# Kernel tuning notes

Hardware: AMD Instinct MI355X
Metric: run time of the kernel (lower is better)

The kernel has to match this reference:

```python
import jax, jax.numpy as jnp
import numpy as np

B, T, D_EMB, D_QKV = 8, 2048, 1024, 64
SCALE = 1.0 / (D_QKV ** 0.5)


def setup_inputs() -> dict:
    key = jax.random.key(0)
    kx, kq, kk, kv = jax.random.split(key, 4)
    return {
        "x": jax.random.normal(kx, (B, T, D_EMB), dtype=jnp.float32),
        "Wq": jax.random.normal(kq, (D_EMB, D_QKV), dtype=jnp.float32) * 0.02,
        "Wk": jax.random.normal(kk, (D_EMB, D_QKV), dtype=jnp.float32) * 0.02,
        "Wv": jax.random.normal(kv, (D_EMB, D_QKV), dtype=jnp.float32) * 0.02,
    }


def reference(x, Wq, Wk, Wv):
    # x: [B, T, D_emb]; projections to [B, T, D_qkv]
    q = jnp.einsum("bte,ed->btd", x, Wq)
    k = jnp.einsum("bte,ed->btd", x, Wk)
    v = jnp.einsum("bte,ed->btd", x, Wv)
    # scores: [B, T, T], scaled then causally masked
    scores = jnp.einsum("bqd,bkd->bqk", q, k) * SCALE
    t = x.shape[1]
    causal = jnp.tril(jnp.ones((t, t), dtype=bool))
    scores = jnp.where(causal[None, :, :], scores, -jnp.inf)
    attn = jax.nn.softmax(scores, axis=-1)
    return jnp.einsum("bqk,bkd->bqd", attn, v)
```

## Files before the change

kernel.cpp:

```cpp
#include <hip/hip_runtime.h>

typedef float f32x4 __attribute__((ext_vector_type(4)));
typedef __bf16 bf16x8 __attribute__((ext_vector_type(8)));
typedef __bf16 bf16x4 __attribute__((ext_vector_type(4)));

#define T_ 2048
#define DE 1024
#define DQ 64
#define SCALE 0.125f

#define GL16(gp, lp)                                                        \
  __builtin_amdgcn_global_load_lds(                                         \
      (const __attribute__((address_space(1))) void*)(gp),                  \
      (__attribute__((address_space(3))) void*)(lp), 16, 0, 0)

#define WAITVM0 asm volatile("s_waitcnt vmcnt(0)" ::: "memory")

__global__ __launch_bounds__(256) void kw_pack(
    const float* __restrict__ Wq, const float* __restrict__ Wk,
    const float* __restrict__ Wv, __bf16* __restrict__ Wf)
{
  int tid = blockIdx.x * 256 + threadIdx.x;
  int lane = tid & 63, f = tid >> 6;
  int t = f % 12, kc = f / 12;
  const float* W = (t < 4) ? Wq : ((t < 8) ? Wk : Wv);
  int nl = (t & 3) * 16 + (lane & 15);
  int k0 = kc * 32 + (lane >> 4) * 8;
  bf16x8 v;
#pragma unroll
  for (int j = 0; j < 8; ++j) v[j] = (__bf16)W[(size_t)(k0 + j) * 64 + nl];
  *(bf16x8*)(Wf + (size_t)tid * 8) = v;
}

__global__ __launch_bounds__(256) void kproj(
    const float* __restrict__ x, const __bf16* __restrict__ Wf,
    __bf16* __restrict__ Qb, __bf16* __restrict__ Kb, __bf16* __restrict__ Vt)
{
  __shared__ char lds[2][32768];
  const int tid = threadIdx.x;
  const int lane = tid & 63;
  const int w = tid >> 6;
  const int col = lane & 15, g = lane >> 4;
  const int msub = w & 1;
  const int ng = w >> 1;
  const int mbase = blockIdx.x * 32;

  size_t gbase[8];
  int gstride[8], ldst[8];
#pragma unroll
  for (int cc = 0; cc < 2; ++cc) {
    int q = w * 2 + cc;
    int row = q * 4 + (lane >> 4);
    int kbyte = ((lane & 15) * 16) ^ ((row & 7) << 4);
    gbase[cc] = (size_t)(mbase + row) * 4096 + (size_t)kbyte;
    gstride[cc] = 256;
    ldst[cc] = q * 1024 + lane * 16;
  }
#pragma unroll
  for (int cc = 2; cc < 8; ++cc) {
    int j = w * 6 + cc - 2;
    gbase[cc] = (size_t)j * 1024 + (size_t)lane * 16;
    gstride[cc] = 24576;
    ldst[cc] = 8192 + j * 1024 + lane * 16;
  }

  f32x4 acc[6];
#pragma unroll
  for (int i = 0; i < 6; ++i) acc[i] = (f32x4){0.f, 0.f, 0.f, 0.f};

  const char* xb = (const char*)x;
  const char* wb = (const char*)Wf;

#define STAGE(ks, bi)                                                       \
  {                                                                         \
    char* lb = &lds[bi][0];                                                 \
    _Pragma("unroll")                                                       \
    for (int cc = 0; cc < 2; ++cc)                                          \
      GL16(xb + gbase[cc] + (size_t)(ks) * gstride[cc], lb + ldst[cc]);     \
    _Pragma("unroll")                                                       \
    for (int cc = 2; cc < 8; ++cc)                                          \
      GL16(wb + gbase[cc] + (size_t)(ks) * gstride[cc], lb + ldst[cc]);     \
  }

#define KSTEP(ks, bi)                                                       \
  {                                                                         \
    const char* la = &lds[bi][0];                                           \
    const char* lbB = &lds[bi][8192];                                       \
    const int arow = msub * 16 + col;                                       \
    const char* abase = la + arow * 256;                                    \
    const int sw = (arow & 7) << 4;                                         \
    _Pragma("unroll")                                                       \
    for (int kh = 0; kh < 2; ++kh) {                                        \
      int kb = kh * 128 + g * 32;                                           \
      f32x4 a0 = *(const f32x4*)(abase + (kb ^ sw));                        \
      f32x4 a1 = *(const f32x4*)(abase + ((kb + 16) ^ sw));                 \
      bf16x8 af;                                                            \
      _Pragma("unroll")                                                     \
      for (int j = 0; j < 4; ++j) { af[j] = (__bf16)a0[j]; af[4 + j] = (__bf16)a1[j]; } \
      _Pragma("unroll")                                                     \
      for (int ii = 0; ii < 6; ++ii) {                                      \
        int nt = ng * 6 + ii;                                               \
        bf16x8 bfr = *(const bf16x8*)(lbB + ((kh * 12 + nt) * 64 + lane) * 16); \
        acc[ii] = __builtin_amdgcn_mfma_f32_16x16x32_bf16(af, bfr, acc[ii], 0, 0, 0); \
      }                                                                     \
    }                                                                       \
  }

  STAGE(0, 0);
  for (int ks = 0; ks < 16; ++ks) {
    WAITVM0;
    __builtin_amdgcn_s_barrier();
    __builtin_amdgcn_sched_barrier(0);
    if (ks < 15) STAGE(ks + 1, (ks + 1) & 1);
    KSTEP(ks, ks & 1);
  }

#undef STAGE
#undef KSTEP

  const int b = mbase >> 11;
  const int mrow = mbase + msub * 16 + g * 4;
  const int trow = (mbase & 2047) + msub * 16 + g * 4;
#pragma unroll
  for (int ii = 0; ii < 6; ++ii) {
    int ti = ng * 6 + ii;
    if (ti < 8) {
      __bf16* dst = (ti < 4) ? Qb : Kb;
      int c = (ti & 3) * 16 + col;
#pragma unroll
      for (int r = 0; r < 4; ++r)
        dst[(size_t)(mrow + r) * DQ + c] = (__bf16)acc[ii][r];
    } else {
      int d = (ti - 8) * 16 + col;
      bf16x4 v;
#pragma unroll
      for (int r = 0; r < 4; ++r) v[r] = (__bf16)acc[ii][r];
      *(bf16x4*)(Vt + ((size_t)(b * DQ + d)) * T_ + trow) = v;
    }
  }
}

__global__ __launch_bounds__(256) void kattn(
    const __bf16* __restrict__ Qb, const __bf16* __restrict__ Kb,
    const __bf16* __restrict__ Vt, float* __restrict__ out)
{
  __shared__ float accs[4][32][68];
  __shared__ float mls[4][2][32];
  __shared__ __bf16 plds[4][2][16][72];

  const int tid = threadIdx.x;
  const int lane = tid & 63;
  const int w = tid >> 6;
  const int col = lane & 15, g = lane >> 4;
  const int b = blockIdx.x & 7;
  const int jq = 63 - (blockIdx.x >> 3);
  const int qbase = jq * 32;

  bf16x8 qa[2][2];
#pragma unroll
  for (int mt = 0; mt < 2; ++mt) {
    const __bf16* Qp = Qb + (size_t)(b * T_ + qbase + mt * 16 + col) * DQ + g * 8;
    qa[mt][0] = *(const bf16x8*)(Qp);
    qa[mt][1] = *(const bf16x8*)(Qp + 32);
  }

  const __bf16* Kbb = Kb + (size_t)b * T_ * DQ;
  const __bf16* Vbb = Vt + (size_t)b * DQ * T_;

  f32x4 acc[2][4];
#pragma unroll
  for (int mt = 0; mt < 2; ++mt)
#pragma unroll
    for (int dt = 0; dt < 4; ++dt) acc[mt][dt] = (f32x4){0.f,0.f,0.f,0.f};
  float mrun[2][4], lsum[2][4];
#pragma unroll
  for (int mt = 0; mt < 2; ++mt)
#pragma unroll
    for (int r = 0; r < 4; ++r) { mrun[mt][r] = -1e30f; lsum[mt][r] = 0.f; }

  const int nb = (jq >> 1) + 1;
  for (int it = w; it < nb; it += 4) {
    const int nbase = it * 64;

    bf16x8 kf_[4][2];
#pragma unroll
    for (int nt = 0; nt < 4; ++nt) {
      const __bf16* Kp = Kbb + (size_t)(nbase + nt * 16 + col) * DQ + g * 8;
      kf_[nt][0] = *(const bf16x8*)(Kp);
      kf_[nt][1] = *(const bf16x8*)(Kp + 32);
    }

    f32x4 s[2][4];
#pragma unroll
    for (int mt = 0; mt < 2; ++mt)
#pragma unroll
      for (int nt = 0; nt < 4; ++nt) {
        f32x4 t = __builtin_amdgcn_mfma_f32_16x16x32_bf16(qa[mt][0], kf_[nt][0],
                                                          (f32x4){0.f,0.f,0.f,0.f}, 0, 0, 0);
        s[mt][nt] = __builtin_amdgcn_mfma_f32_16x16x32_bf16(qa[mt][1], kf_[nt][1], t, 0, 0, 0);
      }

    bf16x8 vf[4][2];
#pragma unroll
    for (int dt = 0; dt < 4; ++dt) {
      const __bf16* Vp = Vbb + (size_t)(dt * 16 + col) * T_ + nbase + g * 8;
      vf[dt][0] = *(const bf16x8*)(Vp);
      vf[dt][1] = *(const bf16x8*)(Vp + 32);
    }

#pragma unroll
    for (int mt = 0; mt < 2; ++mt)
#pragma unroll
      for (int nt = 0; nt < 4; ++nt)
#pragma unroll
        for (int r = 0; r < 4; ++r) s[mt][nt][r] *= SCALE;
    if (it == nb - 1) {
#pragma unroll
      for (int mt = 0; mt < 2; ++mt)
#pragma unroll
        for (int nt = 0; nt < 4; ++nt)
#pragma unroll
          for (int r = 0; r < 4; ++r)
            if (nbase + nt * 16 + col > qbase + mt * 16 + g * 4 + r) s[mt][nt][r] = -1e30f;
    }

    float mv[2][4];
#pragma unroll
    for (int mt = 0; mt < 2; ++mt)
#pragma unroll
      for (int r = 0; r < 4; ++r)
        mv[mt][r] = fmaxf(fmaxf(s[mt][0][r], s[mt][1][r]), fmaxf(s[mt][2][r], s[mt][3][r]));
#pragma unroll
    for (int sh = 1; sh <= 8; sh <<= 1)
#pragma unroll
      for (int mt = 0; mt < 2; ++mt)
#pragma unroll
        for (int r = 0; r < 4; ++r) mv[mt][r] = fmaxf(mv[mt][r], __shfl_xor(mv[mt][r], sh, 64));

#pragma unroll
    for (int mt = 0; mt < 2; ++mt)
#pragma unroll
      for (int r = 0; r < 4; ++r) {
        float mn = fmaxf(mrun[mt][r], mv[mt][r]);
        float rs = __expf(mrun[mt][r] - mn);
        mrun[mt][r] = mn;
        float ps = 0.f;
#pragma unroll
        for (int nt = 0; nt < 4; ++nt) {
          s[mt][nt][r] = __expf(s[mt][nt][r] - mn);
          ps += s[mt][nt][r];
        }
        lsum[mt][r] = lsum[mt][r] * rs + ps;
#pragma unroll
        for (int dt = 0; dt < 4; ++dt) acc[mt][dt][r] *= rs;
      }

#pragma unroll
    for (int mt = 0; mt < 2; ++mt)
#pragma unroll
      for (int nt = 0; nt < 4; ++nt)
#pragma unroll
        for (int r = 0; r < 4; ++r)
          plds[w][mt][g * 4 + r][nt * 16 + col] = (__bf16)s[mt][nt][r];

    bf16x8 pa[2][2];
#pragma unroll
    for (int mt = 0; mt < 2; ++mt) {
      pa[mt][0] = *(const bf16x8*)&plds[w][mt][col][g * 8];
      pa[mt][1] = *(const bf16x8*)&plds[w][mt][col][32 + g * 8];
    }

#pragma unroll
    for (int mt = 0; mt < 2; ++mt)
#pragma unroll
      for (int dt = 0; dt < 4; ++dt) {
        f32x4 t = __builtin_amdgcn_mfma_f32_16x16x32_bf16(pa[mt][0], vf[dt][0], acc[mt][dt], 0, 0, 0);
        acc[mt][dt] = __builtin_amdgcn_mfma_f32_16x16x32_bf16(pa[mt][1], vf[dt][1], t, 0, 0, 0);
      }
  }

#pragma unroll
  for (int sh = 1; sh <= 8; sh <<= 1)
#pragma unroll
    for (int mt = 0; mt < 2; ++mt)
#pragma unroll
      for (int r = 0; r < 4; ++r) lsum[mt][r] += __shfl_xor(lsum[mt][r], sh, 64);

#pragma unroll
  for (int mt = 0; mt < 2; ++mt)
#pragma unroll
    for (int r = 0; r < 4; ++r) {
      int row = mt * 16 + g * 4 + r;
      accs[w][row][col]      = acc[mt][0][r];
      accs[w][row][col + 16] = acc[mt][1][r];
      accs[w][row][col + 32] = acc[mt][2][r];
      accs[w][row][col + 48] = acc[mt][3][r];
      if (col == 0) { mls[w][0][row] = mrun[mt][r]; mls[w][1][row] = lsum[mt][r]; }
    }
  __syncthreads();

#pragma unroll
  for (int pass = 0; pass < 2; ++pass) {
    int row = pass * 16 + (tid >> 4);
    int c4 = (tid & 15) * 4;
    float m0 = mls[0][0][row], m1 = mls[1][0][row];
    float m2 = mls[2][0][row], m3 = mls[3][0][row];
    float M = fmaxf(fmaxf(m0, m1), fmaxf(m2, m3));
    float s0 = __expf(m0 - M), s1 = __expf(m1 - M);
    float s2 = __expf(m2 - M), s3 = __expf(m3 - M);
    float L = s0 * mls[0][1][row] + s1 * mls[1][1][row]
            + s2 * mls[2][1][row] + s3 * mls[3][1][row];
    f32x4 a0 = *(const f32x4*)&accs[0][row][c4];
    f32x4 a1 = *(const f32x4*)&accs[1][row][c4];
    f32x4 a2 = *(const f32x4*)&accs[2][row][c4];
    f32x4 a3 = *(const f32x4*)&accs[3][row][c4];
    float inv = 1.f / L;
    f32x4 o;
#pragma unroll
    for (int j = 0; j < 4; ++j)
      o[j] = (s0 * a0[j] + s1 * a1[j] + s2 * a2[j] + s3 * a3[j]) * inv;
    *(f32x4*)(out + (size_t)(b * T_ + qbase + row) * DQ + c4) = o;
  }
}

extern "C" void kernel_launch(void* const* d_in, const int* in_sizes, int n_in,
                              void* d_out, int out_size, void* d_ws, size_t ws_size,
                              hipStream_t stream)
{
  const float* x  = (const float*)d_in[0];
  const float* Wq = (const float*)d_in[1];
  const float* Wk = (const float*)d_in[2];
  const float* Wv = (const float*)d_in[3];
  float* out = (float*)d_out;

  char* ws = (char*)d_ws;
  __bf16* Wf = (__bf16*)(ws);
  __bf16* Qb = (__bf16*)(ws + 0x80000);
  __bf16* Kb = (__bf16*)(ws + 0x80000 + 0x200000);
  __bf16* Vt = (__bf16*)(ws + 0x80000 + 0x400000);

  kw_pack<<<96, 256, 0, stream>>>(Wq, Wk, Wv, Wf);
  kproj<<<512, 256, 0, stream>>>(x, Wf, Qb, Kb, Vt);
  kattn<<<512, 256, 0, stream>>>(Qb, Kb, Vt, out);
}
```

Before: 51.66 us.

## Triple-buffer x tiles and prefetch two steps ahead in projection kernel

Splits the projection kernel's LDS staging into a 3-deep ring for the x activation tiles and a 2-deep ring for the packed weight tiles. Each iteration waits only until the older loads finish (vmcnt 2) rather than draining all outstanding loads. This lets the x loads for step ks+2 stay in flight while step ks computes, hiding more global latency. The cost is more LDS per block (72KB vs 64KB), which may reduce occupancy, and a fully unrolled loop with fixed wait counts.

```diff
diff --git a/kernel.cpp b/kernel.cpp
--- a/kernel.cpp
+++ b/kernel.cpp
@@ -14,7 +14,7 @@
       (const __attribute__((address_space(1))) void*)(gp),                  \
       (__attribute__((address_space(3))) void*)(lp), 16, 0, 0)
 
-#define WAITVM0 asm volatile("s_waitcnt vmcnt(0)" ::: "memory")
+#define WAITVM(N) asm volatile("s_waitcnt vmcnt(" #N ")" ::: "memory")
 
 __global__ __launch_bounds__(256) void kw_pack(
     const float* __restrict__ Wq, const float* __restrict__ Wk,
@@ -36,7 +36,7 @@
     const float* __restrict__ x, const __bf16* __restrict__ Wf,
     __bf16* __restrict__ Qb, __bf16* __restrict__ Kb, __bf16* __restrict__ Vt)
 {
-  __shared__ char lds[2][32768];
+  __shared__ char lds[3 * 8192 + 2 * 24576];
   const int tid = threadIdx.x;
   const int lane = tid & 63;
   const int w = tid >> 6;
@@ -45,24 +45,19 @@
   const int ng = w >> 1;
   const int mbase = blockIdx.x * 32;
 
-  size_t gbase[8];
-  int gstride[8], ldst[8];
+  size_t gsrcA[2];
+  int ldstA[2];
 #pragma unroll
   for (int cc = 0; cc < 2; ++cc) {
     int q = w * 2 + cc;
     int row = q * 4 + (lane >> 4);
     int kbyte = ((lane & 15) * 16) ^ ((row & 7) << 4);
-    gbase[cc] = (size_t)(mbase + row) * 4096 + (size_t)kbyte;
-    gstride[cc] = 256;
-    ldst[cc] = q * 1024 + lane * 16;
-  }
-#pragma unroll
-  for (int cc = 2; cc < 8; ++cc) {
-    int j = w * 6 + cc - 2;
-    gbase[cc] = (size_t)j * 1024 + (size_t)lane * 16;
-    gstride[cc] = 24576;
-    ldst[cc] = 8192 + j * 1024 + lane * 16;
-  }
+    gsrcA[cc] = (size_t)(mbase + row) * 4096 + (size_t)kbyte;
+    ldstA[cc] = q * 1024 + lane * 16;
+  }
+  int ofsB[6];
+#pragma unroll
+  for (int cc = 0; cc < 6; ++cc) ofsB[cc] = (w * 6 + cc) * 1024 + lane * 16;
 
   f32x4 acc[6];
 #pragma unroll
@@ -71,21 +66,24 @@
   const char* xb = (const char*)x;
   const char* wb = (const char*)Wf;
 
-#define STAGE(ks, bi)                                                       \
+#define STAGE_A(ks)                                                         \
   {                                                                         \
-    char* lb = &lds[bi][0];                                                 \
+    char* lb = &lds[((ks) % 3) * 8192];                                     \
     _Pragma("unroll")                                                       \
     for (int cc = 0; cc < 2; ++cc)                                          \
-      GL16(xb + gbase[cc] + (size_t)(ks) * gstride[cc], lb + ldst[cc]);     \
+      GL16(xb + gsrcA[cc] + (size_t)(ks) * 256, lb + ldstA[cc]);            \
+  }
+#define STAGE_B(ks)                                                         \
+  {                                                                         \
+    char* lb = &lds[24576 + ((ks) & 1) * 24576];                            \
     _Pragma("unroll")                                                       \
-    for (int cc = 2; cc < 8; ++cc)                                          \
-      GL16(wb + gbase[cc] + (size_t)(ks) * gstride[cc], lb + ldst[cc]);     \
-  }
-
-#define KSTEP(ks, bi)                                                       \
+    for (int cc = 0; cc < 6; ++cc)                                          \
+      GL16(wb + (size_t)(ks) * 24576 + ofsB[cc], lb + ofsB[cc]);            \
+  }
+#define KSTEP(ks)                                                           \
   {                                                                         \
-    const char* la = &lds[bi][0];                                           \
-    const char* lbB = &lds[bi][8192];                                       \
+    const char* la = &lds[((ks) % 3) * 8192];                               \
+    const char* lbB = &lds[24576 + ((ks) & 1) * 24576];                     \
     const int arow = msub * 16 + col;                                       \
     const char* abase = la + arow * 256;                                    \
     const int sw = (arow & 7) << 4;                                         \
@@ -105,18 +103,27 @@
       }                                                                     \
     }                                                                       \
   }
-
-  STAGE(0, 0);
-  for (int ks = 0; ks < 16; ++ks) {
-    WAITVM0;
-    __builtin_amdgcn_s_barrier();
-    __builtin_amdgcn_sched_barrier(0);
-    if (ks < 15) STAGE(ks + 1, (ks + 1) & 1);
-    KSTEP(ks, ks & 1);
-  }
-
-#undef STAGE
+#define ITER(ks, vm, doB, doA)                                              \
+  WAITVM(vm);                                                               \
+  __builtin_amdgcn_s_barrier();                                             \
+  __builtin_amdgcn_sched_barrier(0);                                        \
+  if (doB) STAGE_B((ks) + 1);                                               \
+  if (doA) STAGE_A((ks) + 2);                                               \
+  KSTEP(ks);
+
+  STAGE_A(0);
+  STAGE_B(0);
+  STAGE_A(1);
+
+  ITER(0, 2, 1, 1)  ITER(1, 2, 1, 1)  ITER(2, 2, 1, 1)  ITER(3, 2, 1, 1)
+  ITER(4, 2, 1, 1)  ITER(5, 2, 1, 1)  ITER(6, 2, 1, 1)  ITER(7, 2, 1, 1)
+  ITER(8, 2, 1, 1)  ITER(9, 2, 1, 1)  ITER(10, 2, 1, 1) ITER(11, 2, 1, 1)
+  ITER(12, 2, 1, 1) ITER(13, 2, 1, 1) ITER(14, 2, 1, 0) ITER(15, 0, 0, 0)
+
+#undef ITER
 #undef KSTEP
+#undef STAGE_B
+#undef STAGE_A
 
   const int b = mbase >> 11;
   const int mrow = mbase + msub * 16 + g * 4;
```

Result: no change. 50.94 us (-1.4%).
